# Optimization experiments

Measured on AMD Instinct MI355X. Metric: run time of the kernel, lower is better.

## Reference

```python
import jax, jax.numpy as jnp
import numpy as np


def _conv(x, w, b, pad):
    y = jax.lax.conv_general_dilated(
        x, w, window_strides=(1, 1), padding=[(pad, pad), (pad, pad)],
        dimension_numbers=('NCHW', 'OIHW', 'NCHW'))
    return y + b[None, :, None, None]


def _deform_conv2d(x, offsets, mask, w, b):
    # x: [B,C,H,W]; offsets: [B,2*K,H,W] (dy,dx pairs per kernel tap, row-major taps);
    # mask: [B,K,H,W]; w: [O,C,3,3]; stride=1, padding=1 (torchvision semantics).
    B, C, H, W = x.shape
    K = 9
    off = offsets.reshape(B, K, 2, H, W)
    dy, dx = off[:, :, 0], off[:, :, 1]                      # [B,K,H,W]
    ky = (jnp.arange(K) // 3 - 1).astype(x.dtype)            # tap row offset (pad=1)
    kx = (jnp.arange(K) % 3 - 1).astype(x.dtype)             # tap col offset
    hh = jnp.arange(H, dtype=x.dtype)
    ww = jnp.arange(W, dtype=x.dtype)
    py = hh[None, None, :, None] + ky[None, :, None, None] + dy   # sample y, [B,K,H,W]
    px = ww[None, None, None, :] + kx[None, :, None, None] + dx   # sample x
    y0 = jnp.floor(py); x0 = jnp.floor(px)
    wy = py - y0;      wx = px - x0
    y0i = y0.astype(jnp.int32); x0i = x0.astype(jnp.int32)
    xflat = x.reshape(B, C, H * W)

    def gather(yy, xx):
        # zero padding outside the feature map (torchvision behavior)
        valid = ((yy >= 0) & (yy < H) & (xx >= 0) & (xx < W)).astype(x.dtype)
        idx = jnp.clip(yy, 0, H - 1) * W + jnp.clip(xx, 0, W - 1)
        idx = jnp.broadcast_to(idx.reshape(B, 1, K * H * W), (B, C, K * H * W))
        g = jnp.take_along_axis(xflat, idx, axis=2).reshape(B, C, K, H, W)
        return g * valid[:, None]

    sampled = (gather(y0i, x0i)         * ((1 - wy) * (1 - wx))[:, None]
             + gather(y0i, x0i + 1)     * ((1 - wy) * wx)[:, None]
             + gather(y0i + 1, x0i)     * (wy * (1 - wx))[:, None]
             + gather(y0i + 1, x0i + 1) * (wy * wx)[:, None])       # [B,C,K,H,W]
    sampled = sampled * mask[:, None]                                # modulation
    out = jnp.einsum('bckhw,ock->bohw', sampled, w.reshape(w.shape[0], C, K))
    return out + b[None, :, None, None]


def setup_inputs() -> dict:
    key = jax.random.key(0)
    ks = jax.random.split(key, 5)
    B, C, Ht, Wt, Hs, Ws = 4, 256, 32, 32, 64, 64
    return {
        'template_feat': jax.random.normal(ks[0], (B, C, Ht, Wt), jnp.float32),
        'search_feat':   jax.random.normal(ks[1], (B, C, Hs, Ws), jnp.float32),
        'offset_w': jax.random.normal(ks[2], (18, 2 * C, 3, 3), jnp.float32) * 0.01,
        'offset_b': jnp.zeros((18,), jnp.float32),
        'mask_w':   jax.random.normal(ks[3], (9, 2 * C, 1, 1), jnp.float32) * 0.06,
        'mask_b':   jnp.zeros((9,), jnp.float32),
        'deform_w': jax.random.normal(ks[4], (C, C, 3, 3), jnp.float32) * 0.03,
        'deform_b': jnp.zeros((C,), jnp.float32),
    }


def reference(template_feat, search_feat, offset_w, offset_b, mask_w, mask_b, deform_w, deform_b):
    B, C, Hs, Ws = search_feat.shape
    # F.interpolate(..., mode='bilinear', align_corners=False) == jax half-pixel bilinear
    aligned = jax.image.resize(template_feat, (B, C, Hs, Ws), method='bilinear')
    combined = jnp.concatenate([aligned, search_feat], axis=1)       # [B,2C,H,W]
    offsets = _conv(combined, offset_w, offset_b, 1)                 # [B,18,H,W]
    mask = jax.nn.sigmoid(_conv(combined, mask_w, mask_b, 0))        # [B,9,H,W]
    return _deform_conv2d(search_feat, offsets, mask, deform_w, deform_b)
```

## Files before the change

kernel.cpp:

```cpp
#include <hip/hip_runtime.h>
#include <math.h>

#define BB 4
#define CC 256
#define HH 64
#define WW 64
#define HW 4096
#define XTR 4240
#define XPAD 72

typedef __attribute__((ext_vector_type(8))) _Float16 half8;
typedef __attribute__((ext_vector_type(4))) _Float16 half4;
typedef __attribute__((ext_vector_type(4))) float f32x4;

__device__ inline void gld16(const void* g, void* l) {
    __builtin_amdgcn_global_load_lds((const __attribute__((address_space(1))) void*)g,
                                     (__attribute__((address_space(3))) void*)l, 16, 0, 0);
}

__global__ __launch_bounds__(256) void prep_kernel(
    const float* __restrict__ tmpl, const float* __restrict__ search,
    const float* __restrict__ ow, const float* __restrict__ mw,
    const float* __restrict__ dw,
    _Float16* __restrict__ XT, _Float16* __restrict__ W2, _Float16* __restrict__ W3T) {
    int blk = blockIdx.x;
    int tid = threadIdx.x;
    __shared__ _Float16 ts[64 * 72];

    if (blk < 2048) {
        int ct = blk & 7, y = (blk >> 3) & 63, b = blk >> 9;
        if (ct >= 4) {
            const float* sp = search + ((size_t)(b * CC + (ct - 4) * 64) * HW) + y * 64;
#pragma unroll
            for (int it = 0; it < 4; ++it) {
                int c_l = it * 16 + (tid >> 4);
                int x4 = tid & 15;
                float4 v = *(const float4*)(sp + (size_t)c_l * HW + x4 * 4);
                half4 h;
                h.x = (_Float16)v.x; h.y = (_Float16)v.y;
                h.z = (_Float16)v.z; h.w = (_Float16)v.w;
                *(half4*)&ts[c_l * 72 + x4 * 4] = h;
            }
        } else {
            float sy = 0.5f * (float)y - 0.25f;
            float fy = floorf(sy);
            float wy = sy - fy;
            int y0 = (int)fy;
            int y0c = min(max(y0, 0), 31), y1c = min(max(y0 + 1, 0), 31);
            const float* tp0 = tmpl + ((size_t)(b * CC + ct * 64) * 1024);
            for (int it = 0; it < 16; ++it) {
                int c_l = it * 4 + (tid >> 6);
                int x = tid & 63;
                float sx = 0.5f * (float)x - 0.25f;
                float fx = floorf(sx);
                float wx = sx - fx;
                int x0 = (int)fx;
                int x0c = min(max(x0, 0), 31), x1c = min(max(x0 + 1, 0), 31);
                const float* tp = tp0 + (size_t)c_l * 1024;
                float v00 = tp[y0c * 32 + x0c], v01 = tp[y0c * 32 + x1c];
                float v10 = tp[y1c * 32 + x0c], v11 = tp[y1c * 32 + x1c];
                ts[c_l * 72 + x] = (_Float16)((1.f - wy) * ((1.f - wx) * v00 + wx * v01) +
                                              wy * ((1.f - wx) * v10 + wx * v11));
            }
        }
        __syncthreads();
        size_t rowbase = (size_t)b * XTR + XPAD + (size_t)y * 64;
        for (int it = 0; it < 2; ++it) {
            int idx = it * 256 + tid;
            int x = idx >> 3, w = idx & 7;
            half8 o;
#pragma unroll
            for (int j = 0; j < 8; ++j) o[j] = ts[(w * 8 + j) * 72 + x];
            *(half8*)&XT[(rowbase + x) * 512 + ct * 64 + ((w ^ (x & 7)) * 8)] = o;
        }
    } else if (blk < 2192) {
        int idx = (blk - 2048) * 256 + tid;
        int w = idx & 63;
        int r = (idx >> 6) % 144;
        int b = idx / 9216;
        int pr = (r < 72) ? r : (r + 4096);
        half8 z = {};
        *(half8*)&XT[((size_t)b * XTR + pr) * 512 + w * 8] = z;
    } else if (blk < 2264) {
        int idx = (blk - 2192) * 256 + tid;
        int q = idx & 7;
        int oc = (idx >> 3) & 31;
        int tap = (idx >> 8) % 9;
        int ch = idx / 2304;
        int c0 = ch * 64 + (q ^ (oc & 7)) * 8;
        half8 o;
#pragma unroll
        for (int j = 0; j < 8; ++j) {
            int c = c0 + j;
            float v = 0.f;
            if (oc < 18) v = ow[((size_t)oc * 512 + c) * 9 + tap];
            else if (oc < 27 && tap == 4) v = mw[(size_t)(oc - 18) * 512 + c];
            o[j] = (_Float16)v;
        }
        *(half8*)&W2[(size_t)idx * 8] = o;
    } else {
        int g = (blk - 2264) * 256 + tid;
        int ot = g / 36864;
        int rem = g - ot * 36864;
        int ks = rem >> 10;
        int ci = rem & 1023;
        int r = ci >> 3, q = ci & 7;
        int qs = q ^ (r & 7);
        int o_ = ot * 128 + r;
        int kc0 = ks * 64 + qs * 8;
        half8 o;
#pragma unroll
        for (int j = 0; j < 8; ++j) {
            int kc = kc0 + j;
            int k = kc >> 8, c = kc & 255;
            o[j] = (_Float16)dw[((size_t)o_ * CC + c) * 9 + k];
        }
        *(half8*)&W3T[(size_t)g * 8] = o;
    }
}

__global__ __launch_bounds__(512) void offsample_kernel(
    const _Float16* __restrict__ XT, const _Float16* __restrict__ W2,
    const float* __restrict__ ob, const float* __restrict__ mb,
    _Float16* __restrict__ ST2) {
    int blk = blockIdx.x;
    int b = blk >> 6, pt = blk & 63;
    int p0 = pt * 64;
    int tid = threadIdx.x, wave = tid >> 6, lane = tid & 63;
    int l15 = lane & 15, kq = lane >> 4;

    __shared__ __align__(16) _Float16 A_s[18432];
    __shared__ __align__(16) _Float16 B_s[12416];
    __shared__ float offs_s[27 * 64];
    __shared__ ushort4 r4[576];
    __shared__ float4 wg4[576];

    f32x4 acc[2];
    acc[0] = (f32x4){0.f, 0.f, 0.f, 0.f};
    acc[1] = (f32x4){0.f, 0.f, 0.f, 0.f};

    const char* xrow = (const char*)(XT + ((size_t)b * XTR + XPAD + p0 - 65) * 512);
    half8 z8 = {};
    int x_ = (wave & 3) * 16 + l15;

    for (int ch = 0; ch < 8; ++ch) {
        __syncthreads();
        if (tid < 256) {
            const char* srcA = (const char*)W2 + (size_t)ch * 36864;
#pragma unroll
            for (int it = 0; it < 9; ++it) {
                int b16 = it * 256 + wave * 64;
                gld16(srcA + (size_t)(b16 + lane) * 16, (char*)A_s + b16 * 16);
            }
#pragma unroll
            for (int it = 0; it < 7; ++it) {
                int b16 = it * 256 + wave * 64;
                if (b16 < 1552) {
                    int c16 = b16 + lane;
                    int r_u = c16 >> 3, q = c16 & 7;
                    gld16(xrow + (size_t)r_u * 1024 + ch * 128 + q * 16, (char*)B_s + b16 * 16);
                }
            }
        }
        __syncthreads();

        if (tid < 256) {
#pragma unroll
            for (int tap = 0; tap < 9; ++tap) {
                int ky = tap / 3 - 1, kx = tap % 3 - 1;
                int dlt = ky * 64 + kx;
                int key = (l15 + dlt + 72) & 7;
                bool iv0 = (kx == -1 && x_ == 0) || (kx == 1 && x_ == 63);
                int r0 = wave * 16 + l15 + 65 + dlt;
#pragma unroll
                for (int ks = 0; ks < 2; ++ks) {
                    int qa = ((ks * 4 + kq) ^ (l15 & 7)) * 8;
                    int qb = ((ks * 4 + kq) ^ key) * 8;
                    half8 fa0 = *(const half8*)&A_s[tap * 2048 + l15 * 64 + qa];
                    half8 fa1 = *(const half8*)&A_s[tap * 2048 + (16 + l15) * 64 + qa];
                    half8 fb0 = *(const half8*)&B_s[r0 * 64 + qb];
                    if (iv0) fb0 = z8;
                    acc[0] = __builtin_amdgcn_mfma_f32_16x16x32_f16(fa0, fb0, acc[0], 0, 0, 0);
                    acc[1] = __builtin_amdgcn_mfma_f32_16x16x32_f16(fa1, fb0, acc[1], 0, 0, 0);
                }
            }
        }
    }

    if (tid < 256) {
#pragma unroll
        for (int m = 0; m < 2; ++m) {
#pragma unroll
            for (int r = 0; r < 4; ++r) {
                int oc = m * 16 + kq * 4 + r;
                float v = acc[m][r];
                if (oc < 18) {
                    offs_s[oc * 64 + x_] = v + ob[oc];
                } else if (oc < 27) {
                    float s = v + mb[oc - 18];
                    offs_s[oc * 64 + x_] = 1.f / (1.f + expf(-s));
                }
            }
        }
    }
    __syncthreads();

    for (int i = tid; i < 576; i += 512) {
        int k = i >> 6, t = i & 63;
        int p = p0 + t;
        int y = p >> 6, x = p & 63;
        float dy = offs_s[(2 * k) * 64 + t];
        float dx = offs_s[(2 * k + 1) * 64 + t];
        float m = offs_s[(18 + k) * 64 + t];
        float py = (float)(y + k / 3 - 1) + dy;
        float px = (float)(x + k % 3 - 1) + dx;
        float fy0 = floorf(py), fx0 = floorf(px);
        float wy = py - fy0, wx = px - fx0;
        int y0 = (int)fy0, x0 = (int)fx0;
        bool vy0 = (y0 >= 0) && (y0 < HH);
        bool vy1 = (y0 + 1 >= 0) && (y0 + 1 < HH);
        bool vx0 = (x0 >= 0) && (x0 < WW);
        bool vx1 = (x0 + 1 >= 0) && (x0 + 1 < WW);
        float w00 = (vy0 && vx0) ? (1.f - wy) * (1.f - wx) * m : 0.f;
        float w01 = (vy0 && vx1) ? (1.f - wy) * wx * m : 0.f;
        float w10 = (vy1 && vx0) ? wy * (1.f - wx) * m : 0.f;
        float w11 = (vy1 && vx1) ? wy * wx * m : 0.f;
        int y0c = min(max(y0, 0), HH - 1), y1c = min(max(y0 + 1, 0), HH - 1);
        int x0c = min(max(x0, 0), WW - 1), x1c = min(max(x0 + 1, 0), WW - 1);
        r4[i] = make_ushort4((ushort)(y0c * 64 + x0c), (ushort)(y0c * 64 + x1c),
                             (ushort)(y1c * 64 + x0c), (ushort)(y1c * 64 + x1c));
        wg4[i] = make_float4(w00, w01, w10, w11);
    }
    __syncthreads();

    const _Float16* xb = XT + ((size_t)b * XTR + XPAD) * 512;
    int oct = tid & 31;
    int gg64 = (4 + (oct >> 3)) * 64;
    int w0 = oct & 7;
    size_t tb = ((size_t)(b * 32 + (pt >> 1))) * 36;
    int rbase = (pt & 1) * 64;

    for (int k = 0; k < 9; ++k) {
        int ks36 = k * 4 + (oct >> 3);
#pragma unroll
        for (int it = 0; it < 4; ++it) {
            int p_l = it * 16 + (tid >> 5);
            ushort4 rr = r4[k * 64 + p_l];
            float4 w = wg4[k * 64 + p_l];
            half8 c00 = *(const half8*)(xb + (size_t)rr.x * 512 + gg64 + ((w0 ^ (rr.x & 7)) * 8));
            half8 c01 = *(const half8*)(xb + (size_t)rr.y * 512 + gg64 + ((w0 ^ (rr.y & 7)) * 8));
            half8 c10 = *(const half8*)(xb + (size_t)rr.z * 512 + gg64 + ((w0 ^ (rr.z & 7)) * 8));
            half8 c11 = *(const half8*)(xb + (size_t)rr.w * 512 + gg64 + ((w0 ^ (rr.w & 7)) * 8));
            half8 o;
#pragma unroll
            for (int j = 0; j < 8; ++j) {
                float v = w.x * (float)c00[j] + w.y * (float)c01[j] +
                          w.z * (float)c10[j] + w.w * (float)c11[j];
                o[j] = (_Float16)v;
            }
            int r = rbase + p_l;
            *(half8*)&ST2[((tb + ks36) << 13) + (r * 8 + (w0 ^ (r & 7))) * 8] = o;
        }
    }
}

__global__ __launch_bounds__(512) void deform_mfma(
    const _Float16* __restrict__ W3T, const _Float16* __restrict__ ST2,
    const float* __restrict__ db, float* __restrict__ out) {
    int blk = blockIdx.x;
    int b = blk >> 6;
    int ot = (blk >> 5) & 1;
    int pt = blk & 31;
    int o0 = ot * 128, p0 = pt * 128;
    int tid = threadIdx.x;
    int wave = tid >> 6, lane = tid & 63;
    int wo = (wave & 1) * 64, wp = (wave >> 1) * 32;

    __shared__ __align__(16) _Float16 As[4][8192];
    __shared__ __align__(16) _Float16 Bs[4][8192];

    f32x4 acc[4][2];
#pragma unroll
    for (int i = 0; i < 4; ++i)
#pragma unroll
        for (int j = 0; j < 2; ++j) acc[i][j] = (f32x4){0.f, 0.f, 0.f, 0.f};

    const _Float16* Asrc = W3T + (size_t)ot * (36 * 8192);
    const _Float16* Bsrc = ST2 + ((size_t)(b * 32 + pt)) * (36 * 8192);
    int fr = lane & 15, kq8 = lane >> 4;

    auto stage = [&](int buf, int ks) {
#pragma unroll
        for (int t = 0; t < 2; ++t) {
            int ci = t * 512 + tid;
            gld16(Asrc + (((size_t)ks) << 13) + (size_t)ci * 8,
                  (char*)&As[buf][0] + (size_t)ci * 16);
        }
#pragma unroll
        for (int t = 0; t < 2; ++t) {
            int ci = t * 512 + tid;
            gld16(Bsrc + (((size_t)ks) << 13) + (size_t)ci * 8,
                  (char*)&Bs[buf][0] + (size_t)ci * 16);
        }
    };

    auto compute = [&](int cur) {
        __builtin_amdgcn_s_setprio(1);
#pragma unroll
        for (int ks2 = 0; ks2 < 2; ++ks2) {
            int c8 = ks2 * 4 + kq8;
            int cho = (c8 ^ (fr & 7)) * 8;
            half8 fa[4], fb[2];
#pragma unroll
            for (int f = 0; f < 4; ++f)
                fa[f] = *(const half8*)&As[cur][(wo + f * 16 + fr) * 64 + cho];
#pragma unroll
            for (int g = 0; g < 2; ++g)
                fb[g] = *(const half8*)&Bs[cur][(wp + g * 16 + fr) * 64 + cho];
#pragma unroll
            for (int i = 0; i < 4; ++i)
#pragma unroll
                for (int j = 0; j < 2; ++j)
                    acc[i][j] = __builtin_amdgcn_mfma_f32_16x16x32_f16(fa[i], fb[j], acc[i][j], 0, 0, 0);
        }
        __builtin_amdgcn_s_setprio(0);
    };

    stage(0, 0);
    stage(1, 1);
    stage(2, 2);

    for (int m = 0; m < 8; ++m) {
#pragma unroll
        for (int u = 0; u < 4; ++u) {
            int ks = m * 4 + u;
            asm volatile("s_waitcnt vmcnt(8)" ::: "memory");
            __builtin_amdgcn_s_barrier();
            asm volatile("" ::: "memory");
            compute(u);
            stage((u + 3) & 3, ks + 3);
        }
    }
    asm volatile("s_waitcnt vmcnt(8)" ::: "memory");
    __builtin_amdgcn_s_barrier();
    asm volatile("" ::: "memory");
    compute(0);
    stage(3, 35);
    asm volatile("s_waitcnt vmcnt(8)" ::: "memory");
    __builtin_amdgcn_s_barrier();
    asm volatile("" ::: "memory");
    compute(1);
    asm volatile("s_waitcnt vmcnt(4)" ::: "memory");
    __builtin_amdgcn_s_barrier();
    asm volatile("" ::: "memory");
    compute(2);
    asm volatile("s_waitcnt vmcnt(0)" ::: "memory");
    __builtin_amdgcn_s_barrier();
    asm volatile("" ::: "memory");
    compute(3);

    int col = lane & 15, rb = (lane >> 4) * 4;
#pragma unroll
    for (int i = 0; i < 4; ++i) {
        int o_ = o0 + wo + i * 16 + rb;
#pragma unroll
        for (int j = 0; j < 2; ++j) {
            int p_ = p0 + wp + j * 16 + col;
#pragma unroll
            for (int r = 0; r < 4; ++r) {
                out[((size_t)(b * CC + o_ + r)) * HW + p_] = acc[i][j][r] + db[o_ + r];
            }
        }
    }
}

extern "C" void kernel_launch(void* const* d_in, const int* in_sizes, int n_in,
                              void* d_out, int out_size, void* d_ws, size_t ws_size,
                              hipStream_t stream) {
    const float* tmpl = (const float*)d_in[0];
    const float* search = (const float*)d_in[1];
    const float* ow = (const float*)d_in[2];
    const float* ob = (const float*)d_in[3];
    const float* mw = (const float*)d_in[4];
    const float* mb = (const float*)d_in[5];
    const float* dw = (const float*)d_in[6];
    const float* db = (const float*)d_in[7];
    float* out = (float*)d_out;

    _Float16* XTp = (_Float16*)d_ws;
    _Float16* W2 = XTp + (size_t)4 * XTR * 512;
    _Float16* W3T = W2 + 147456;
    _Float16* ST2 = W3T + 589824;

    prep_kernel<<<2552, 256, 0, stream>>>(tmpl, search, ow, mw, dw, XTp, W2, W3T);
    offsample_kernel<<<256, 512, 0, stream>>>(XTp, W2, ob, mb, ST2);
    deform_mfma<<<256, 512, 0, stream>>>(W3T, ST2, db, out);
}
```

Baseline: 82.35 us.

## Split offset/mask conv and bilinear sampling into separate kernels

The fused offset-conv-plus-sampling kernel is split in two. An MFMA kernel with 256 threads computes the offsets and sigmoid masks and writes them to global memory. A separate sampling kernel then runs twice as many blocks, each covering 32 pixels, to do the bilinear gather. This gives the gather-heavy sampling more parallelism and removes the idle half-block during the conv. The cost is an extra launch plus a global round-trip for the offsets and masks.

```diff
diff --git a/kernel.cpp b/kernel.cpp
--- a/kernel.cpp
+++ b/kernel.cpp
@@ -119,10 +119,10 @@
     }
 }
 
-__global__ __launch_bounds__(512) void offsample_kernel(
+__global__ __launch_bounds__(256) void offmask_mfma(
     const _Float16* __restrict__ XT, const _Float16* __restrict__ W2,
     const float* __restrict__ ob, const float* __restrict__ mb,
-    _Float16* __restrict__ ST2) {
+    float* __restrict__ offs, float* __restrict__ maskv) {
     int blk = blockIdx.x;
     int b = blk >> 6, pt = blk & 63;
     int p0 = pt * 64;
@@ -131,9 +131,6 @@
 
     __shared__ __align__(16) _Float16 A_s[18432];
     __shared__ __align__(16) _Float16 B_s[12416];
-    __shared__ float offs_s[27 * 64];
-    __shared__ ushort4 r4[576];
-    __shared__ float4 wg4[576];
 
     f32x4 acc[2];
     acc[0] = (f32x4){0.f, 0.f, 0.f, 0.f};
@@ -141,77 +138,83 @@
 
     const char* xrow = (const char*)(XT + ((size_t)b * XTR + XPAD + p0 - 65) * 512);
     half8 z8 = {};
-    int x_ = (wave & 3) * 16 + l15;
+    int x_ = wave * 16 + l15;
 
     for (int ch = 0; ch < 8; ++ch) {
         __syncthreads();
-        if (tid < 256) {
-            const char* srcA = (const char*)W2 + (size_t)ch * 36864;
-#pragma unroll
-            for (int it = 0; it < 9; ++it) {
-                int b16 = it * 256 + wave * 64;
-                gld16(srcA + (size_t)(b16 + lane) * 16, (char*)A_s + b16 * 16);
-            }
-#pragma unroll
-            for (int it = 0; it < 7; ++it) {
-                int b16 = it * 256 + wave * 64;
-                if (b16 < 1552) {
-                    int c16 = b16 + lane;
-                    int r_u = c16 >> 3, q = c16 & 7;
-                    gld16(xrow + (size_t)r_u * 1024 + ch * 128 + q * 16, (char*)B_s + b16 * 16);
-                }
+        const char* srcA = (const char*)W2 + (size_t)ch * 36864;
+#pragma unroll
+        for (int it = 0; it < 9; ++it) {
+            int b16 = it * 256 + wave * 64;
+            gld16(srcA + (size_t)(b16 + lane) * 16, (char*)A_s + b16 * 16);
+        }
+#pragma unroll
+        for (int it = 0; it < 7; ++it) {
+            int b16 = it * 256 + wave * 64;
+            if (b16 < 1552) {
+                int c16 = b16 + lane;
+                int r_u = c16 >> 3, q = c16 & 7;
+                gld16(xrow + (size_t)r_u * 1024 + ch * 128 + q * 16, (char*)B_s + b16 * 16);
             }
         }
         __syncthreads();
 
-        if (tid < 256) {
-#pragma unroll
-            for (int tap = 0; tap < 9; ++tap) {
-                int ky = tap / 3 - 1, kx = tap % 3 - 1;
-                int dlt = ky * 64 + kx;
-                int key = (l15 + dlt + 72) & 7;
-                bool iv0 = (kx == -1 && x_ == 0) || (kx == 1 && x_ == 63);
-                int r0 = wave * 16 + l15 + 65 + dlt;
-#pragma unroll
-                for (int ks = 0; ks < 2; ++ks) {
-                    int qa = ((ks * 4 + kq) ^ (l15 & 7)) * 8;
-                    int qb = ((ks * 4 + kq) ^ key) * 8;
-                    half8 fa0 = *(const half8*)&A_s[tap * 2048 + l15 * 64 + qa];
-                    half8 fa1 = *(const half8*)&A_s[tap * 2048 + (16 + l15) * 64 + qa];
-                    half8 fb0 = *(const half8*)&B_s[r0 * 64 + qb];
-                    if (iv0) fb0 = z8;
-                    acc[0] = __builtin_amdgcn_mfma_f32_16x16x32_f16(fa0, fb0, acc[0], 0, 0, 0);
-                    acc[1] = __builtin_amdgcn_mfma_f32_16x16x32_f16(fa1, fb0, acc[1], 0, 0, 0);
-                }
-            }
-        }
-    }
-
-    if (tid < 256) {
-#pragma unroll
-        for (int m = 0; m < 2; ++m) {
-#pragma unroll
-            for (int r = 0; r < 4; ++r) {
-                int oc = m * 16 + kq * 4 + r;
-                float v = acc[m][r];
-                if (oc < 18) {
-                    offs_s[oc * 64 + x_] = v + ob[oc];
-                } else if (oc < 27) {
-                    float s = v + mb[oc - 18];
-                    offs_s[oc * 64 + x_] = 1.f / (1.f + expf(-s));
-                }
-            }
-        }
-    }
-    __syncthreads();
-
-    for (int i = tid; i < 576; i += 512) {
-        int k = i >> 6, t = i & 63;
+#pragma unroll
+        for (int tap = 0; tap < 9; ++tap) {
+            int ky = tap / 3 - 1, kx = tap % 3 - 1;
+            int dlt = ky * 64 + kx;
+            int key = (l15 + dlt + 72) & 7;
+            bool iv0 = (kx == -1 && x_ == 0) || (kx == 1 && x_ == 63);
+            int r0 = wave * 16 + l15 + 65 + dlt;
+#pragma unroll
+            for (int ks = 0; ks < 2; ++ks) {
+                int qa = ((ks * 4 + kq) ^ (l15 & 7)) * 8;
+                int qb = ((ks * 4 + kq) ^ key) * 8;
+                half8 fa0 = *(const half8*)&A_s[tap * 2048 + l15 * 64 + qa];
+                half8 fa1 = *(const half8*)&A_s[tap * 2048 + (16 + l15) * 64 + qa];
+                half8 fb0 = *(const half8*)&B_s[r0 * 64 + qb];
+                if (iv0) fb0 = z8;
+                acc[0] = __builtin_amdgcn_mfma_f32_16x16x32_f16(fa0, fb0, acc[0], 0, 0, 0);
+                acc[1] = __builtin_amdgcn_mfma_f32_16x16x32_f16(fa1, fb0, acc[1], 0, 0, 0);
+            }
+        }
+    }
+
+    int px = p0 + x_;
+#pragma unroll
+    for (int m = 0; m < 2; ++m) {
+#pragma unroll
+        for (int r = 0; r < 4; ++r) {
+            int oc = m * 16 + kq * 4 + r;
+            float v = acc[m][r];
+            if (oc < 18) {
+                offs[(size_t)(b * 18 + oc) * HW + px] = v + ob[oc];
+            } else if (oc < 27) {
+                float s = v + mb[oc - 18];
+                maskv[(size_t)(b * 9 + oc - 18) * HW + px] = 1.f / (1.f + expf(-s));
+            }
+        }
+    }
+}
+
+__global__ __launch_bounds__(512) void sample_kernel(
+    const _Float16* __restrict__ XT, const float* __restrict__ offs,
+    const float* __restrict__ maskv, _Float16* __restrict__ ST2) {
+    int blk = blockIdx.x;
+    int b = blk >> 7, pt = blk & 127;
+    int p0 = pt * 32;
+    int tid = threadIdx.x;
+
+    __shared__ ushort4 r4[288];
+    __shared__ float4 wg4[288];
+
+    for (int i = tid; i < 288; i += 512) {
+        int k = i >> 5, t = i & 31;
         int p = p0 + t;
         int y = p >> 6, x = p & 63;
-        float dy = offs_s[(2 * k) * 64 + t];
-        float dx = offs_s[(2 * k + 1) * 64 + t];
-        float m = offs_s[(18 + k) * 64 + t];
+        float dy = offs[((size_t)(b * 18 + 2 * k)) * HW + p];
+        float dx = offs[((size_t)(b * 18 + 2 * k + 1)) * HW + p];
+        float m = maskv[((size_t)(b * 9 + k)) * HW + p];
         float py = (float)(y + k / 3 - 1) + dy;
         float px = (float)(x + k % 3 - 1) + dx;
         float fy0 = floorf(py), fx0 = floorf(px);
@@ -237,16 +240,16 @@
     int oct = tid & 31;
     int gg64 = (4 + (oct >> 3)) * 64;
     int w0 = oct & 7;
-    size_t tb = ((size_t)(b * 32 + (pt >> 1))) * 36;
-    int rbase = (pt & 1) * 64;
+    size_t tb = ((size_t)(b * 32 + (pt >> 2))) * 36;
+    int rbase = (pt & 3) * 32;
 
     for (int k = 0; k < 9; ++k) {
         int ks36 = k * 4 + (oct >> 3);
 #pragma unroll
-        for (int it = 0; it < 4; ++it) {
+        for (int it = 0; it < 2; ++it) {
             int p_l = it * 16 + (tid >> 5);
-            ushort4 rr = r4[k * 64 + p_l];
-            float4 w = wg4[k * 64 + p_l];
+            ushort4 rr = r4[k * 32 + p_l];
+            float4 w = wg4[k * 32 + p_l];
             half8 c00 = *(const half8*)(xb + (size_t)rr.x * 512 + gg64 + ((w0 ^ (rr.x & 7)) * 8));
             half8 c01 = *(const half8*)(xb + (size_t)rr.y * 512 + gg64 + ((w0 ^ (rr.y & 7)) * 8));
             half8 c10 = *(const half8*)(xb + (size_t)rr.z * 512 + gg64 + ((w0 ^ (rr.z & 7)) * 8));
@@ -391,8 +394,11 @@
     _Float16* W2 = XTp + (size_t)4 * XTR * 512;
     _Float16* W3T = W2 + 147456;
     _Float16* ST2 = W3T + 589824;
+    float* offsv = (float*)(ST2 + 37748736);
+    float* maskv = offsv + 294912;
 
     prep_kernel<<<2552, 256, 0, stream>>>(tmpl, search, ow, mw, dw, XTp, W2, W3T);
-    offsample_kernel<<<256, 512, 0, stream>>>(XTp, W2, ob, mb, ST2);
+    offmask_mfma<<<256, 256, 0, stream>>>(XTp, W2, ob, mb, offsv, maskv);
+    sample_kernel<<<BB * 128, 512, 0, stream>>>(XTp, offsv, maskv, ST2);
     deform_mfma<<<256, 512, 0, stream>>>(W3T, ST2, db, out);
 }
```

New measurement: 85.82 us. 4.2% more time.

## Split offset-conv channel chunks across both wave groups with LDS reduction

Applied to the files above, without the earlier changes.

The offset/mask convolution stage previously used only the first 4 of 8 waves, looping over 8 channel chunks. Now both 4-wave groups each handle half the chunks with separate LDS staging buffers, and the partial accumulators are summed through shared memory before the sigmoid and offset epilogue. This aims to halve the serial MFMA and load loop in this stage. In exchange it raises LDS use to about 122 KB per block, which limits occupancy, and adds an extra reduction step with barriers.

```diff
diff --git a/kernel.cpp b/kernel.cpp
--- a/kernel.cpp
+++ b/kernel.cpp
@@ -128,12 +128,17 @@
     int p0 = pt * 64;
     int tid = threadIdx.x, wave = tid >> 6, lane = tid & 63;
     int l15 = lane & 15, kq = lane >> 4;
-
-    __shared__ __align__(16) _Float16 A_s[18432];
-    __shared__ __align__(16) _Float16 B_s[12416];
-    __shared__ float offs_s[27 * 64];
-    __shared__ ushort4 r4[576];
-    __shared__ float4 wg4[576];
+    int grp = wave >> 2;
+    int w4 = wave & 3;
+    int tid256 = tid & 255;
+
+    __shared__ __align__(16) char smem[124928];
+    _Float16* A_s = (_Float16*)(smem + grp * 62464);
+    _Float16* B_s = (_Float16*)(smem + grp * 62464 + 36864);
+    float* red_s = (float*)smem;
+    float* offs_s = (float*)(smem + 8192);
+    ushort4* r4 = (ushort4*)(smem + 15104);
+    float4* wg4 = (float4*)(smem + 19712);
 
     f32x4 acc[2];
     acc[0] = (f32x4){0.f, 0.f, 0.f, 0.f};
@@ -141,59 +146,65 @@
 
     const char* xrow = (const char*)(XT + ((size_t)b * XTR + XPAD + p0 - 65) * 512);
     half8 z8 = {};
-    int x_ = (wave & 3) * 16 + l15;
-
-    for (int ch = 0; ch < 8; ++ch) {
+    int x_ = w4 * 16 + l15;
+
+    for (int ch4 = 0; ch4 < 4; ++ch4) {
+        int ch = grp * 4 + ch4;
         __syncthreads();
-        if (tid < 256) {
-            const char* srcA = (const char*)W2 + (size_t)ch * 36864;
-#pragma unroll
-            for (int it = 0; it < 9; ++it) {
-                int b16 = it * 256 + wave * 64;
-                gld16(srcA + (size_t)(b16 + lane) * 16, (char*)A_s + b16 * 16);
-            }
-#pragma unroll
-            for (int it = 0; it < 7; ++it) {
-                int b16 = it * 256 + wave * 64;
-                if (b16 < 1552) {
-                    int c16 = b16 + lane;
-                    int r_u = c16 >> 3, q = c16 & 7;
-                    gld16(xrow + (size_t)r_u * 1024 + ch * 128 + q * 16, (char*)B_s + b16 * 16);
-                }
+        const char* srcA = (const char*)W2 + (size_t)ch * 36864;
+#pragma unroll
+        for (int it = 0; it < 9; ++it) {
+            int b16 = it * 256 + w4 * 64;
+            gld16(srcA + (size_t)(b16 + lane) * 16, (char*)A_s + b16 * 16);
+        }
+#pragma unroll
+        for (int it = 0; it < 7; ++it) {
+            int b16 = it * 256 + w4 * 64;
+            if (b16 < 1552) {
+                int c16 = b16 + lane;
+                int r_u = c16 >> 3, q = c16 & 7;
+                gld16(xrow + (size_t)r_u * 1024 + ch * 128 + q * 16, (char*)B_s + b16 * 16);
             }
         }
         __syncthreads();
 
-        if (tid < 256) {
-#pragma unroll
-            for (int tap = 0; tap < 9; ++tap) {
-                int ky = tap / 3 - 1, kx = tap % 3 - 1;
-                int dlt = ky * 64 + kx;
-                int key = (l15 + dlt + 72) & 7;
-                bool iv0 = (kx == -1 && x_ == 0) || (kx == 1 && x_ == 63);
-                int r0 = wave * 16 + l15 + 65 + dlt;
-#pragma unroll
-                for (int ks = 0; ks < 2; ++ks) {
-                    int qa = ((ks * 4 + kq) ^ (l15 & 7)) * 8;
-                    int qb = ((ks * 4 + kq) ^ key) * 8;
-                    half8 fa0 = *(const half8*)&A_s[tap * 2048 + l15 * 64 + qa];
-                    half8 fa1 = *(const half8*)&A_s[tap * 2048 + (16 + l15) * 64 + qa];
-                    half8 fb0 = *(const half8*)&B_s[r0 * 64 + qb];
-                    if (iv0) fb0 = z8;
-                    acc[0] = __builtin_amdgcn_mfma_f32_16x16x32_f16(fa0, fb0, acc[0], 0, 0, 0);
-                    acc[1] = __builtin_amdgcn_mfma_f32_16x16x32_f16(fa1, fb0, acc[1], 0, 0, 0);
-                }
-            }
-        }
-    }
-
-    if (tid < 256) {
+#pragma unroll
+        for (int tap = 0; tap < 9; ++tap) {
+            int ky = tap / 3 - 1, kx = tap % 3 - 1;
+            int dlt = ky * 64 + kx;
+            int key = (l15 + dlt + 72) & 7;
+            bool iv0 = (kx == -1 && x_ == 0) || (kx == 1 && x_ == 63);
+            int r0 = w4 * 16 + l15 + 65 + dlt;
+#pragma unroll
+            for (int ks = 0; ks < 2; ++ks) {
+                int qa = ((ks * 4 + kq) ^ (l15 & 7)) * 8;
+                int qb = ((ks * 4 + kq) ^ key) * 8;
+                half8 fa0 = *(const half8*)&A_s[tap * 2048 + l15 * 64 + qa];
+                half8 fa1 = *(const half8*)&A_s[tap * 2048 + (16 + l15) * 64 + qa];
+                half8 fb0 = *(const half8*)&B_s[r0 * 64 + qb];
+                if (iv0) fb0 = z8;
+                acc[0] = __builtin_amdgcn_mfma_f32_16x16x32_f16(fa0, fb0, acc[0], 0, 0, 0);
+                acc[1] = __builtin_amdgcn_mfma_f32_16x16x32_f16(fa1, fb0, acc[1], 0, 0, 0);
+            }
+        }
+    }
+
+    __syncthreads();
+    if (grp == 1) {
+#pragma unroll
+        for (int m = 0; m < 2; ++m)
+#pragma unroll
+            for (int r = 0; r < 4; ++r)
+                red_s[(m * 4 + r) * 256 + tid256] = acc[m][r];
+    }
+    __syncthreads();
+    if (grp == 0) {
 #pragma unroll
         for (int m = 0; m < 2; ++m) {
 #pragma unroll
             for (int r = 0; r < 4; ++r) {
                 int oc = m * 16 + kq * 4 + r;
-                float v = acc[m][r];
+                float v = acc[m][r] + red_s[(m * 4 + r) * 256 + tid256];
                 if (oc < 18) {
                     offs_s[oc * 64 + x_] = v + ob[oc];
                 } else if (oc < 27) {
```

Result: faster. 80.17 us (-2.6%).
